# Performance work log

Measured on AMD Instinct MI355X. Metric: run time of the kernel, lower is better.

## Reference

```python
import jax, jax.numpy as jnp
import numpy as np

N_NODES = 100000
N_EDGES = 3200000
IN_CH = 512
OUT_CH = 64


def setup_inputs() -> dict:
    key = jax.random.key(0)
    k1, k2, k3 = jax.random.split(key, 3)
    edge_index = jax.random.randint(k1, (2, N_EDGES), 0, N_NODES, dtype=jnp.int64)
    x = jax.random.normal(k2, (N_NODES, IN_CH), dtype=jnp.float32)
    W = jax.random.normal(k3, (IN_CH, OUT_CH), dtype=jnp.float32)
    return {"edge_index": edge_index, "x": x, "W": W}


def _propagate(h, row, col, norm, self_norm):
    # one hop of normalized adjacency: (D^-1/2 (A+I) D^-1/2) @ h
    msg = jax.ops.segment_sum(norm[:, None] * h[col], row, num_segments=h.shape[0])
    return msg + self_norm[:, None] * h


def reference(edge_index, x, W):
    n = x.shape[0]
    row, col = edge_index[0], edge_index[1]
    # remove_self_loops then add_self_loops: mask out i==i edges, add identity
    loop_mask = (row != col).astype(x.dtype)
    deg = jax.ops.segment_sum(loop_mask, row, num_segments=n) + 1.0  # +1 self-loop
    dinv = jax.lax.rsqrt(deg)  # deg >= 1, never inf
    norm = dinv[row] * dinv[col] * loop_mask
    self_norm = dinv * dinv
    # A_hat^2 @ (x W) == A_hat @ (A_hat @ (x W)); avoids sparse-sparse matmul
    h = x @ W
    h = _propagate(h, row, col, norm, self_norm)
    h = _propagate(h, row, col, norm, self_norm)
    return h
```

## Files before the change

kernel.cpp:

```cpp
#include <hip/hip_runtime.h>
#include <hip/hip_bf16.h>


#define OUTC 64
#define INC 512
#define ELLW 72
#define RPB 128
#define NBUCK 782
#define PBLK 256
#define CAP 32
#define OVFCAP 65536

typedef short bf16x8 __attribute__((ext_vector_type(8)));
typedef float f32x4 __attribute__((ext_vector_type(4)));
typedef int i32x4 __attribute__((ext_vector_type(4)));

static __device__ inline short f2bf(float f) {
    union { __hip_bfloat16 b; short s; } u;
    u.b = __float2bfloat16(f);
    return u.s;
}
static __device__ inline float bf2f(unsigned short s) {
    union { float f; unsigned u; } v;
    v.u = ((unsigned)s) << 16;
    return v.f;
}

__global__ __launch_bounds__(1024) void bucket_scatter(const int* __restrict__ erow,
                                                       int* __restrict__ cnt_pb,
                                                       unsigned int* __restrict__ buf,
                                                       unsigned long long* __restrict__ ovf,
                                                       int* __restrict__ ovf_cnt,
                                                       int nE, int n) {
    __shared__ int lcnt[NBUCK];
    for (int i = threadIdx.x; i < NBUCK; i += 1024) lcnt[i] = 0;
    __syncthreads();
    const int blk = blockIdx.x;
    const int chunk = nE / PBLK;
    const int e0 = blk * chunk;
    const int e1 = (blk == PBLK - 1) ? nE : e0 + chunk;
    const int q0 = e0 >> 2, q1 = e1 >> 2;
    const i32x4* rows4 = (const i32x4*)erow;
    const i32x4* cols4 = (const i32x4*)(erow + nE);
    for (int q = q0 + (int)threadIdx.x; q < q1; q += 1024) {
        i32x4 r4 = __builtin_nontemporal_load(&rows4[q]);
        i32x4 c4 = __builtin_nontemporal_load(&cols4[q]);
#pragma unroll
        for (int k = 0; k < 4; ++k) {
            int r = r4[k], c = c4[k];
            if (r == c) continue;
            int b = r >> 7;
            int p = atomicAdd(&lcnt[b], 1);
            if (p < CAP) {
                buf[((size_t)b * PBLK + blk) * CAP + p] =
                    ((unsigned int)(r & (RPB - 1)) << 17) | (unsigned int)c;
            } else {
                int qq = atomicAdd(ovf_cnt, 1);
                if (qq < OVFCAP)
                    ovf[qq] = ((unsigned long long)(unsigned)r << 32) | (unsigned)c;
            }
        }
    }
    for (int e = (q1 << 2) + (int)threadIdx.x; e < e1; e += 1024) {
        int r = erow[e], c = erow[nE + e];
        if (r == c) continue;
        int b = r >> 7;
        int p = atomicAdd(&lcnt[b], 1);
        if (p < CAP) {
            buf[((size_t)b * PBLK + blk) * CAP + p] =
                ((unsigned int)(r & (RPB - 1)) << 17) | (unsigned int)c;
        } else {
            int qq = atomicAdd(ovf_cnt, 1);
            if (qq < OVFCAP)
                ovf[qq] = ((unsigned long long)(unsigned)r << 32) | (unsigned)c;
        }
    }
    __syncthreads();
    for (int i = threadIdx.x; i < NBUCK; i += 1024) {
        int v = lcnt[i];
        cnt_pb[(size_t)i * PBLK + blk] = v < CAP ? v : CAP;
    }
}

__global__ __launch_bounds__(256) void ell_from_buckets(const unsigned int* __restrict__ buf,
                                                        const int* __restrict__ cnt_pb,
                                                        const unsigned long long* __restrict__ ovf,
                                                        const int* __restrict__ ovf_cnt,
                                                        int* __restrict__ cnt,
                                                        float* __restrict__ dinv,
                                                        int* __restrict__ ell, int n) {
    __shared__ int segc[PBLK];
    __shared__ int rcnt[RPB];
    __shared__ int slab[RPB * ELLW];
    const int b = blockIdx.x;
    for (int i = threadIdx.x; i < PBLK; i += 256) segc[i] = cnt_pb[(size_t)b * PBLK + i];
    for (int i = threadIdx.x; i < RPB; i += 256) rcnt[i] = 0;
    __syncthreads();
    const unsigned int* bb = buf + (size_t)b * PBLK * CAP;
    const int TOT = PBLK * CAP;
    for (int j = threadIdx.x; j < TOT; j += 256) {
        int s = j >> 5;
        int off = j & (CAP - 1);
        if (off < segc[s]) {
            unsigned int u = bb[j];
            int lr = (int)(u >> 17);
            int c = (int)(u & 0x1FFFFu);
            int p = atomicAdd(&rcnt[lr], 1);
            if (p < ELLW) slab[lr * ELLW + p] = c;
        }
    }
    int m = *ovf_cnt;
    if (m > OVFCAP) m = OVFCAP;
    for (int i = threadIdx.x; i < m; i += 256) {
        unsigned long long e = ovf[i];
        int r = (int)(e >> 32);
        if ((r >> 7) == b) {
            int lr = r & (RPB - 1);
            int p = atomicAdd(&rcnt[lr], 1);
            if (p < ELLW) slab[lr * ELLW + p] = (int)(unsigned)(e & 0xFFFFFFFFu);
        }
    }
    __syncthreads();
    for (int lr = threadIdx.x; lr < RPB; lr += 256) {
        int r = b * RPB + lr;
        if (r < n) {
            int d = rcnt[lr];
            cnt[r] = d;
            dinv[r] = rsqrtf((float)d + 1.0f);
        }
    }
    int* dst = ell + (size_t)b * RPB * ELLW;
    for (int i = threadIdx.x; i < RPB * ELLW; i += 256) dst[i] = slab[i];
}

__global__ __launch_bounds__(256) void prep_w(const float* __restrict__ W,
                                              short* __restrict__ Whp,
                                              short* __restrict__ Wlp) {
    const int tid = blockIdx.x * 256 + threadIdx.x;
    const int lane = tid & 63;
    const int frag = tid >> 6;
    const int kt = frag >> 2;
    const int nt = frag & 3;
    const int col = nt * 16 + (lane & 15);
    const int kb = kt * 32 + (lane >> 4) * 8;
    short h8[8], l8[8];
#pragma unroll
    for (int j = 0; j < 8; ++j) {
        float w = W[(size_t)(kb + j) * OUTC + col];
        short wh = f2bf(w);
        h8[j] = wh;
        l8[j] = f2bf(w - bf2f((unsigned short)wh));
    }
    size_t o = ((size_t)frag * 64 + lane) * 8;
#pragma unroll
    for (int j = 0; j < 8; ++j) { Whp[o + j] = h8[j]; Wlp[o + j] = l8[j]; }
}

__global__ __launch_bounds__(256) void gemm_mfma(const float* __restrict__ x,
                                                 const short* __restrict__ Whp,
                                                 const short* __restrict__ Wlp,
                                                 const float* __restrict__ dinv,
                                                 unsigned short* __restrict__ h, int n) {
    const int lane = threadIdx.x & 63;
    const int wid = __builtin_amdgcn_readfirstlane(threadIdx.x >> 6);
    const int m0 = (blockIdx.x * 4 + wid) * 16;
    if (m0 >= n) return;
    const int quad = lane >> 4;
    const int row = m0 + (lane & 15);

    f32x4 acc[4];
#pragma unroll
    for (int nt = 0; nt < 4; ++nt) acc[nt] = (f32x4){0.f, 0.f, 0.f, 0.f};

    const float* xrow = x + (size_t)row * INC + quad * 8;

    for (int kt = 0; kt < 16; ++kt) {
        float4 a0 = *(const float4*)(xrow + kt * 32);
        float4 a1 = *(const float4*)(xrow + kt * 32 + 4);
        float av[8] = {a0.x, a0.y, a0.z, a0.w, a1.x, a1.y, a1.z, a1.w};
        bf16x8 ah, al;
#pragma unroll
        for (int j = 0; j < 8; ++j) {
            short hj = f2bf(av[j]);
            ah[j] = hj;
            al[j] = f2bf(av[j] - bf2f((unsigned short)hj));
        }
        const size_t fb = ((size_t)kt * 4 * 64 + lane) * 8;
#pragma unroll
        for (int nt = 0; nt < 4; ++nt) {
            bf16x8 bh = *(const bf16x8*)&Whp[fb + (size_t)nt * 64 * 8];
            bf16x8 bl = *(const bf16x8*)&Wlp[fb + (size_t)nt * 64 * 8];
            acc[nt] = __builtin_amdgcn_mfma_f32_16x16x32_bf16(ah, bh, acc[nt], 0, 0, 0);
            acc[nt] = __builtin_amdgcn_mfma_f32_16x16x32_bf16(ah, bl, acc[nt], 0, 0, 0);
            acc[nt] = __builtin_amdgcn_mfma_f32_16x16x32_bf16(al, bh, acc[nt], 0, 0, 0);
        }
    }
    float dv[4];
#pragma unroll
    for (int reg = 0; reg < 4; ++reg) dv[reg] = dinv[m0 + quad * 4 + reg];
#pragma unroll
    for (int nt = 0; nt < 4; ++nt) {
#pragma unroll
        for (int reg = 0; reg < 4; ++reg) {
            int crow = m0 + quad * 4 + reg;
            h[(size_t)crow * OUTC + nt * 16 + (lane & 15)] =
                (unsigned short)f2bf(dv[reg] * acc[nt][reg]);
        }
    }
}

__global__ __launch_bounds__(256) void prop_ell(const unsigned short* __restrict__ hs,
                                                void* __restrict__ hout,
                                                const int* __restrict__ cnt,
                                                const int* __restrict__ ell,
                                                const float* __restrict__ dinv,
                                                int n, int finalhop) {
    const int lane = threadIdx.x & 63;
    const int wid = __builtin_amdgcn_readfirstlane(threadIdx.x >> 6);
    const int node = blockIdx.x * 4 + wid;
    if (node >= n) return;
    float acc = bf2f(hs[(size_t)node * OUTC + lane]);
    int deg = cnt[node];
    if (deg > ELLW) deg = ELLW;
    const int* rowp = ell + (size_t)node * ELLW;
    int j = 0;
    for (; j + 16 <= deg; j += 16) {
        int4 c0 = *(const int4*)(rowp + j);
        int4 c1 = *(const int4*)(rowp + j + 4);
        int4 c2 = *(const int4*)(rowp + j + 8);
        int4 c3 = *(const int4*)(rowp + j + 12);
        float t0 = bf2f(hs[(size_t)c0.x * OUTC + lane]);
        float t1 = bf2f(hs[(size_t)c0.y * OUTC + lane]);
        float t2 = bf2f(hs[(size_t)c0.z * OUTC + lane]);
        float t3 = bf2f(hs[(size_t)c0.w * OUTC + lane]);
        float t4 = bf2f(hs[(size_t)c1.x * OUTC + lane]);
        float t5 = bf2f(hs[(size_t)c1.y * OUTC + lane]);
        float t6 = bf2f(hs[(size_t)c1.z * OUTC + lane]);
        float t7 = bf2f(hs[(size_t)c1.w * OUTC + lane]);
        float t8 = bf2f(hs[(size_t)c2.x * OUTC + lane]);
        float t9 = bf2f(hs[(size_t)c2.y * OUTC + lane]);
        float ta = bf2f(hs[(size_t)c2.z * OUTC + lane]);
        float tb = bf2f(hs[(size_t)c2.w * OUTC + lane]);
        float tc = bf2f(hs[(size_t)c3.x * OUTC + lane]);
        float td = bf2f(hs[(size_t)c3.y * OUTC + lane]);
        float te = bf2f(hs[(size_t)c3.z * OUTC + lane]);
        float tf = bf2f(hs[(size_t)c3.w * OUTC + lane]);
        acc += ((t0 + t1) + (t2 + t3)) + ((t4 + t5) + (t6 + t7));
        acc += ((t8 + t9) + (ta + tb)) + ((tc + td) + (te + tf));
    }
    for (; j + 4 <= deg; j += 4) {
        int4 c0 = *(const int4*)(rowp + j);
        float t0 = bf2f(hs[(size_t)c0.x * OUTC + lane]);
        float t1 = bf2f(hs[(size_t)c0.y * OUTC + lane]);
        float t2 = bf2f(hs[(size_t)c0.z * OUTC + lane]);
        float t3 = bf2f(hs[(size_t)c0.w * OUTC + lane]);
        acc += (t0 + t1) + (t2 + t3);
    }
    for (; j < deg; ++j) {
        int cc = rowp[j];
        acc += bf2f(hs[(size_t)cc * OUTC + lane]);
    }
    float di = dinv[node];
    if (finalhop) {
        ((float*)hout)[(size_t)node * OUTC + lane] = di * acc;
    } else {
        ((unsigned short*)hout)[(size_t)node * OUTC + lane] =
            (unsigned short)f2bf(di * di * acc);
    }
}

extern "C" void kernel_launch(void* const* d_in, const int* in_sizes, int n_in,
                              void* d_out, int out_size, void* d_ws, size_t ws_size,
                              hipStream_t stream) {
    const int n = out_size / OUTC;
    const int nE = in_sizes[0] / 2;
    const int* erow = (const int*)d_in[0];
    const float* x = (const float*)d_in[1];
    const float* W = (const float*)d_in[2];
    float* out = (float*)d_out;

    char* base = (char*)d_ws;
    size_t off = 0;
    auto take = [&](size_t nbytes) -> void* {
        void* p = base + off;
        off += (nbytes + 255) & ~(size_t)255;
        return p;
    };
    int* cnt = (int*)take((size_t)n * 4);
    float* dinv = (float*)take((size_t)n * 4);
    int* ell = (int*)take((size_t)NBUCK * RPB * ELLW * 4);
    short* Whp = (short*)take((size_t)INC * OUTC * 2);
    short* Wlp = (short*)take((size_t)INC * OUTC * 2);
    unsigned short* h0 = (unsigned short*)take((size_t)n * OUTC * 2);
    unsigned short* h1 = (unsigned short*)take((size_t)n * OUTC * 2);
    unsigned int* buf = (unsigned int*)take((size_t)NBUCK * PBLK * CAP * 4);
    int* cnt_pb = (int*)take((size_t)NBUCK * PBLK * 4);
    unsigned long long* ovf = (unsigned long long*)take((size_t)OVFCAP * 8);
    int* ovf_cnt = (int*)take(256);

    (void)hipMemsetAsync(ovf_cnt, 0, 4, stream);

    bucket_scatter<<<PBLK, 1024, 0, stream>>>(erow, cnt_pb, buf, ovf, ovf_cnt, nE, n);

    ell_from_buckets<<<NBUCK, 256, 0, stream>>>(buf, cnt_pb, ovf, ovf_cnt, cnt, dinv, ell, n);

    prep_w<<<16, 256, 0, stream>>>(W, Whp, Wlp);

    const int nwaves = (n + 15) / 16;
    gemm_mfma<<<(nwaves + 3) / 4, 256, 0, stream>>>(x, Whp, Wlp, dinv, h0, n);

    prop_ell<<<(n + 3) / 4, 256, 0, stream>>>(h0, (void*)h1, cnt, ell, dinv, n, 0);
    prop_ell<<<(n + 3) / 4, 256, 0, stream>>>(h1, (void*)out, cnt, ell, dinv, n, 1);
}
```

Before: 497.5 us.

## Partition propagation gather into column segments for cache locality

The ELL construction now sorts each row's neighbours into four source-node ranges and stores per-segment counts. Propagation runs as four passes per hop, each gathering only from one quarter of the feature rows so that pass's working set can stay in cache. Partial sums go to an fp32 accumulator buffer in global memory. This adds extra read-modify-write traffic on the accumulator, more kernel launches, and a second scan over the buckets during ELL construction.

```diff
diff --git a/kernel.cpp b/kernel.cpp
--- a/kernel.cpp
+++ b/kernel.cpp
@@ -10,6 +10,7 @@
 #define PBLK 256
 #define CAP 32
 #define OVFCAP 65536
+#define NSEG 4
 
 typedef short bf16x8 __attribute__((ext_vector_type(8)));
 typedef float f32x4 __attribute__((ext_vector_type(4)));
@@ -25,6 +26,7 @@
     v.u = ((unsigned)s) << 16;
     return v.f;
 }
+
 
 __global__ __launch_bounds__(1024) void bucket_scatter(const int* __restrict__ erow,
                                                        int* __restrict__ cnt_pb,
@@ -86,27 +88,28 @@
                                                         const int* __restrict__ cnt_pb,
                                                         const unsigned long long* __restrict__ ovf,
                                                         const int* __restrict__ ovf_cnt,
-                                                        int* __restrict__ cnt,
+                                                        int4* __restrict__ cnt4,
                                                         float* __restrict__ dinv,
-                                                        int* __restrict__ ell, int n) {
+                                                        int* __restrict__ ell,
+                                                        int n, int segw) {
     __shared__ int segc[PBLK];
-    __shared__ int rcnt[RPB];
+    __shared__ int scnt[RPB][NSEG];
+    __shared__ int soff[RPB][NSEG];
+    __shared__ int scur[RPB][NSEG];
     __shared__ int slab[RPB * ELLW];
     const int b = blockIdx.x;
     for (int i = threadIdx.x; i < PBLK; i += 256) segc[i] = cnt_pb[(size_t)b * PBLK + i];
-    for (int i = threadIdx.x; i < RPB; i += 256) rcnt[i] = 0;
+    for (int i = threadIdx.x; i < RPB * NSEG; i += 256) ((int*)scnt)[i] = 0;
     __syncthreads();
     const unsigned int* bb = buf + (size_t)b * PBLK * CAP;
     const int TOT = PBLK * CAP;
     for (int j = threadIdx.x; j < TOT; j += 256) {
-        int s = j >> 5;
-        int off = j & (CAP - 1);
+        int s = j >> 5, off = j & (CAP - 1);
         if (off < segc[s]) {
             unsigned int u = bb[j];
             int lr = (int)(u >> 17);
             int c = (int)(u & 0x1FFFFu);
-            int p = atomicAdd(&rcnt[lr], 1);
-            if (p < ELLW) slab[lr * ELLW + p] = c;
+            atomicAdd(&scnt[lr][c / segw], 1);
         }
     }
     int m = *ovf_cnt;
@@ -115,18 +118,61 @@
         unsigned long long e = ovf[i];
         int r = (int)(e >> 32);
         if ((r >> 7) == b) {
+            int c = (int)(unsigned)(e & 0xFFFFFFFFu);
+            atomicAdd(&scnt[r & (RPB - 1)][c / segw], 1);
+        }
+    }
+    __syncthreads();
+    for (int lr = threadIdx.x; lr < RPB; lr += 256) {
+        int o = 0;
+#pragma unroll
+        for (int s = 0; s < NSEG; ++s) {
+            soff[lr][s] = o < ELLW ? o : ELLW;
+            scur[lr][s] = 0;
+            o += scnt[lr][s];
+        }
+    }
+    __syncthreads();
+    for (int j = threadIdx.x; j < TOT; j += 256) {
+        int s = j >> 5, off = j & (CAP - 1);
+        if (off < segc[s]) {
+            unsigned int u = bb[j];
+            int lr = (int)(u >> 17);
+            int c = (int)(u & 0x1FFFFu);
+            int sg = c / segw;
+            int p = atomicAdd(&scur[lr][sg], 1);
+            int idx = soff[lr][sg] + p;
+            if (idx < ELLW) slab[lr * ELLW + idx] = c;
+        }
+    }
+    for (int i = threadIdx.x; i < m; i += 256) {
+        unsigned long long e = ovf[i];
+        int r = (int)(e >> 32);
+        if ((r >> 7) == b) {
             int lr = r & (RPB - 1);
-            int p = atomicAdd(&rcnt[lr], 1);
-            if (p < ELLW) slab[lr * ELLW + p] = (int)(unsigned)(e & 0xFFFFFFFFu);
+            int c = (int)(unsigned)(e & 0xFFFFFFFFu);
+            int sg = c / segw;
+            int p = atomicAdd(&scur[lr][sg], 1);
+            int idx = soff[lr][sg] + p;
+            if (idx < ELLW) slab[lr * ELLW + idx] = c;
         }
     }
     __syncthreads();
     for (int lr = threadIdx.x; lr < RPB; lr += 256) {
         int r = b * RPB + lr;
         if (r < n) {
-            int d = rcnt[lr];
-            cnt[r] = d;
-            dinv[r] = rsqrtf((float)d + 1.0f);
+            int raw = scnt[lr][0] + scnt[lr][1] + scnt[lr][2] + scnt[lr][3];
+            int pl[NSEG];
+#pragma unroll
+            for (int s = 0; s < NSEG; ++s) {
+                int start = soff[lr][s];
+                int avail = ELLW - start;
+                if (avail < 0) avail = 0;
+                int p = scnt[lr][s];
+                pl[s] = p < avail ? p : avail;
+            }
+            cnt4[r] = make_int4(pl[0], pl[1], pl[2], pl[3]);
+            dinv[r] = rsqrtf((float)raw + 1.0f);
         }
     }
     int* dst = ell + (size_t)b * RPB * ELLW;
@@ -156,6 +202,7 @@
     for (int j = 0; j < 8; ++j) { Whp[o + j] = h8[j]; Wlp[o + j] = l8[j]; }
 }
 
+
 __global__ __launch_bounds__(256) void gemm_mfma(const float* __restrict__ x,
                                                  const short* __restrict__ Whp,
                                                  const short* __restrict__ Wlp,
@@ -209,63 +256,54 @@
     }
 }
 
-__global__ __launch_bounds__(256) void prop_ell(const unsigned short* __restrict__ hs,
+__global__ __launch_bounds__(256) void prop_seg(const unsigned short* __restrict__ hs,
+                                                float* __restrict__ acc,
                                                 void* __restrict__ hout,
-                                                const int* __restrict__ cnt,
+                                                const int4* __restrict__ cnt4,
                                                 const int* __restrict__ ell,
                                                 const float* __restrict__ dinv,
-                                                int n, int finalhop) {
+                                                int n, int seg, int finalhop) {
     const int lane = threadIdx.x & 63;
     const int wid = __builtin_amdgcn_readfirstlane(threadIdx.x >> 6);
     const int node = blockIdx.x * 4 + wid;
     if (node >= n) return;
-    float acc = bf2f(hs[(size_t)node * OUTC + lane]);
-    int deg = cnt[node];
-    if (deg > ELLW) deg = ELLW;
-    const int* rowp = ell + (size_t)node * ELLW;
+    int4 c4 = cnt4[node];
+    int cs[4] = {c4.x, c4.y, c4.z, c4.w};
+    int start = 0;
+    for (int s = 0; s < seg; ++s) start += cs[s];
+    const int len = cs[seg];
+    const int* rowp = ell + (size_t)node * ELLW + start;
+    float a = 0.f;
     int j = 0;
-    for (; j + 16 <= deg; j += 16) {
-        int4 c0 = *(const int4*)(rowp + j);
-        int4 c1 = *(const int4*)(rowp + j + 4);
-        int4 c2 = *(const int4*)(rowp + j + 8);
-        int4 c3 = *(const int4*)(rowp + j + 12);
-        float t0 = bf2f(hs[(size_t)c0.x * OUTC + lane]);
-        float t1 = bf2f(hs[(size_t)c0.y * OUTC + lane]);
-        float t2 = bf2f(hs[(size_t)c0.z * OUTC + lane]);
-        float t3 = bf2f(hs[(size_t)c0.w * OUTC + lane]);
-        float t4 = bf2f(hs[(size_t)c1.x * OUTC + lane]);
-        float t5 = bf2f(hs[(size_t)c1.y * OUTC + lane]);
-        float t6 = bf2f(hs[(size_t)c1.z * OUTC + lane]);
-        float t7 = bf2f(hs[(size_t)c1.w * OUTC + lane]);
-        float t8 = bf2f(hs[(size_t)c2.x * OUTC + lane]);
-        float t9 = bf2f(hs[(size_t)c2.y * OUTC + lane]);
-        float ta = bf2f(hs[(size_t)c2.z * OUTC + lane]);
-        float tb = bf2f(hs[(size_t)c2.w * OUTC + lane]);
-        float tc = bf2f(hs[(size_t)c3.x * OUTC + lane]);
-        float td = bf2f(hs[(size_t)c3.y * OUTC + lane]);
-        float te = bf2f(hs[(size_t)c3.z * OUTC + lane]);
-        float tf = bf2f(hs[(size_t)c3.w * OUTC + lane]);
-        acc += ((t0 + t1) + (t2 + t3)) + ((t4 + t5) + (t6 + t7));
-        acc += ((t8 + t9) + (ta + tb)) + ((tc + td) + (te + tf));
-    }
-    for (; j + 4 <= deg; j += 4) {
-        int4 c0 = *(const int4*)(rowp + j);
-        float t0 = bf2f(hs[(size_t)c0.x * OUTC + lane]);
-        float t1 = bf2f(hs[(size_t)c0.y * OUTC + lane]);
-        float t2 = bf2f(hs[(size_t)c0.z * OUTC + lane]);
-        float t3 = bf2f(hs[(size_t)c0.w * OUTC + lane]);
-        acc += (t0 + t1) + (t2 + t3);
-    }
-    for (; j < deg; ++j) {
-        int cc = rowp[j];
-        acc += bf2f(hs[(size_t)cc * OUTC + lane]);
-    }
-    float di = dinv[node];
-    if (finalhop) {
-        ((float*)hout)[(size_t)node * OUTC + lane] = di * acc;
+    for (; j + 8 <= len; j += 8) {
+        int i0 = rowp[j], i1 = rowp[j + 1], i2 = rowp[j + 2], i3 = rowp[j + 3];
+        int i4 = rowp[j + 4], i5 = rowp[j + 5], i6 = rowp[j + 6], i7 = rowp[j + 7];
+        float t0 = bf2f(hs[(size_t)i0 * OUTC + lane]);
+        float t1 = bf2f(hs[(size_t)i1 * OUTC + lane]);
+        float t2 = bf2f(hs[(size_t)i2 * OUTC + lane]);
+        float t3 = bf2f(hs[(size_t)i3 * OUTC + lane]);
+        float t4 = bf2f(hs[(size_t)i4 * OUTC + lane]);
+        float t5 = bf2f(hs[(size_t)i5 * OUTC + lane]);
+        float t6 = bf2f(hs[(size_t)i6 * OUTC + lane]);
+        float t7 = bf2f(hs[(size_t)i7 * OUTC + lane]);
+        a += ((t0 + t1) + (t2 + t3)) + ((t4 + t5) + (t6 + t7));
+    }
+    for (; j < len; ++j)
+        a += bf2f(hs[(size_t)rowp[j] * OUTC + lane]);
+
+    const size_t oi = (size_t)node * OUTC + lane;
+    if (seg == 0) {
+        a += bf2f(hs[oi]);
+        acc[oi] = a;
+    } else if (seg < NSEG - 1) {
+        acc[oi] += a;
     } else {
-        ((unsigned short*)hout)[(size_t)node * OUTC + lane] =
-            (unsigned short)f2bf(di * di * acc);
+        float v = acc[oi] + a;
+        float di = dinv[node];
+        if (finalhop)
+            ((float*)hout)[oi] = di * v;
+        else
+            ((unsigned short*)hout)[oi] = (unsigned short)f2bf(di * di * v);
     }
 }
 
@@ -278,6 +316,7 @@
     const float* x = (const float*)d_in[1];
     const float* W = (const float*)d_in[2];
     float* out = (float*)d_out;
+    const int segw = (n + NSEG - 1) / NSEG;
 
     char* base = (char*)d_ws;
     size_t off = 0;
@@ -286,13 +325,14 @@
         off += (nbytes + 255) & ~(size_t)255;
         return p;
     };
-    int* cnt = (int*)take((size_t)n * 4);
+    int4* cnt4 = (int4*)take((size_t)n * 16);
     float* dinv = (float*)take((size_t)n * 4);
     int* ell = (int*)take((size_t)NBUCK * RPB * ELLW * 4);
     short* Whp = (short*)take((size_t)INC * OUTC * 2);
     short* Wlp = (short*)take((size_t)INC * OUTC * 2);
     unsigned short* h0 = (unsigned short*)take((size_t)n * OUTC * 2);
     unsigned short* h1 = (unsigned short*)take((size_t)n * OUTC * 2);
+    float* acc = (float*)take((size_t)n * OUTC * 4);
     unsigned int* buf = (unsigned int*)take((size_t)NBUCK * PBLK * CAP * 4);
     int* cnt_pb = (int*)take((size_t)NBUCK * PBLK * 4);
     unsigned long long* ovf = (unsigned long long*)take((size_t)OVFCAP * 8);
@@ -301,14 +341,16 @@
     (void)hipMemsetAsync(ovf_cnt, 0, 4, stream);
 
     bucket_scatter<<<PBLK, 1024, 0, stream>>>(erow, cnt_pb, buf, ovf, ovf_cnt, nE, n);
-
-    ell_from_buckets<<<NBUCK, 256, 0, stream>>>(buf, cnt_pb, ovf, ovf_cnt, cnt, dinv, ell, n);
-
+    ell_from_buckets<<<NBUCK, 256, 0, stream>>>(buf, cnt_pb, ovf, ovf_cnt, cnt4, dinv,
+                                                ell, n, segw);
     prep_w<<<16, 256, 0, stream>>>(W, Whp, Wlp);
 
     const int nwaves = (n + 15) / 16;
     gemm_mfma<<<(nwaves + 3) / 4, 256, 0, stream>>>(x, Whp, Wlp, dinv, h0, n);
 
-    prop_ell<<<(n + 3) / 4, 256, 0, stream>>>(h0, (void*)h1, cnt, ell, dinv, n, 0);
-    prop_ell<<<(n + 3) / 4, 256, 0, stream>>>(h1, (void*)out, cnt, ell, dinv, n, 1);
-}
+    const int pgrid = (n + 3) / 4;
+    for (int s = 0; s < NSEG; ++s)
+        prop_seg<<<pgrid, 256, 0, stream>>>(h0, acc, (void*)h1, cnt4, ell, dinv, n, s, 0);
+    for (int s = 0; s < NSEG; ++s)
+        prop_seg<<<pgrid, 256, 0, stream>>>(h1, acc, (void*)out, cnt4, ell, dinv, n, s, 1);
+}
```

Result: slower. 740.8 us (+48.9%).

## Co-schedule edge bucketing with the GEMM in one launch and defer dinv scaling

Applied to the files above, without the earlier changes.

The edge bucket scatter and the x@W MFMA GEMM now run as one kernel whose blocks split by index, so the atomic-bound scatter overlaps the bandwidth-bound GEMM. Because dinv is not known yet when the GEMM runs, the dinv row scaling of h0 moves into ell_from_buckets, which rescales each row slab in place after computing degrees. Nontemporal loads and stores are also added in the GEMM and propagation kernels. This costs an extra read-modify-write pass over h0 and a second bf16 rounding, and the scatter blocks drop from 1024 to 512 threads.

```diff
diff --git a/kernel.cpp b/kernel.cpp
--- a/kernel.cpp
+++ b/kernel.cpp
@@ -10,10 +10,12 @@
 #define PBLK 256
 #define CAP 32
 #define OVFCAP 65536
+#define GEMM_BLK 782
 
 typedef short bf16x8 __attribute__((ext_vector_type(8)));
 typedef float f32x4 __attribute__((ext_vector_type(4)));
 typedef int i32x4 __attribute__((ext_vector_type(4)));
+typedef unsigned short u16x4 __attribute__((ext_vector_type(4)));
 
 static __device__ inline short f2bf(float f) {
     union { __hip_bfloat16 b; short s; } u;
@@ -26,28 +28,71 @@
     return v.f;
 }
 
-__global__ __launch_bounds__(1024) void bucket_scatter(const int* __restrict__ erow,
-                                                       int* __restrict__ cnt_pb,
-                                                       unsigned int* __restrict__ buf,
-                                                       unsigned long long* __restrict__ ovf,
-                                                       int* __restrict__ ovf_cnt,
-                                                       int nE, int n) {
-    __shared__ int lcnt[NBUCK];
-    for (int i = threadIdx.x; i < NBUCK; i += 1024) lcnt[i] = 0;
-    __syncthreads();
-    const int blk = blockIdx.x;
-    const int chunk = nE / PBLK;
-    const int e0 = blk * chunk;
-    const int e1 = (blk == PBLK - 1) ? nE : e0 + chunk;
-    const int q0 = e0 >> 2, q1 = e1 >> 2;
-    const i32x4* rows4 = (const i32x4*)erow;
-    const i32x4* cols4 = (const i32x4*)(erow + nE);
-    for (int q = q0 + (int)threadIdx.x; q < q1; q += 1024) {
-        i32x4 r4 = __builtin_nontemporal_load(&rows4[q]);
-        i32x4 c4 = __builtin_nontemporal_load(&cols4[q]);
-#pragma unroll
-        for (int k = 0; k < 4; ++k) {
-            int r = r4[k], c = c4[k];
+__global__ __launch_bounds__(256) void prep_w(const float* __restrict__ W,
+                                              short* __restrict__ Whp,
+                                              short* __restrict__ Wlp) {
+    const int tid = blockIdx.x * 256 + threadIdx.x;
+    const int lane = tid & 63;
+    const int frag = tid >> 6;
+    const int kt = frag >> 2;
+    const int nt = frag & 3;
+    const int col = nt * 16 + (lane & 15);
+    const int kb = kt * 32 + (lane >> 4) * 8;
+    short h8[8], l8[8];
+#pragma unroll
+    for (int j = 0; j < 8; ++j) {
+        float w = W[(size_t)(kb + j) * OUTC + col];
+        short wh = f2bf(w);
+        h8[j] = wh;
+        l8[j] = f2bf(w - bf2f((unsigned short)wh));
+    }
+    size_t o = ((size_t)frag * 64 + lane) * 8;
+#pragma unroll
+    for (int j = 0; j < 8; ++j) { Whp[o + j] = h8[j]; Wlp[o + j] = l8[j]; }
+}
+
+__global__ __launch_bounds__(512) void scatter_and_gemm(const int* __restrict__ erow,
+                                                        int* __restrict__ cnt_pb,
+                                                        unsigned int* __restrict__ buf,
+                                                        unsigned long long* __restrict__ ovf,
+                                                        int* __restrict__ ovf_cnt,
+                                                        const float* __restrict__ x,
+                                                        const short* __restrict__ Whp,
+                                                        const short* __restrict__ Wlp,
+                                                        unsigned short* __restrict__ h,
+                                                        int nE, int n) {
+    if (blockIdx.x < PBLK) {
+        __shared__ int lcnt[NBUCK];
+        for (int i = threadIdx.x; i < NBUCK; i += 512) lcnt[i] = 0;
+        __syncthreads();
+        const int blk = blockIdx.x;
+        const int chunk = nE / PBLK;
+        const int e0 = blk * chunk;
+        const int e1 = (blk == PBLK - 1) ? nE : e0 + chunk;
+        const int q0 = e0 >> 2, q1 = e1 >> 2;
+        const i32x4* rows4 = (const i32x4*)erow;
+        const i32x4* cols4 = (const i32x4*)(erow + nE);
+        for (int q = q0 + (int)threadIdx.x; q < q1; q += 512) {
+            i32x4 r4 = __builtin_nontemporal_load(&rows4[q]);
+            i32x4 c4 = __builtin_nontemporal_load(&cols4[q]);
+#pragma unroll
+            for (int k = 0; k < 4; ++k) {
+                int r = r4[k], c = c4[k];
+                if (r == c) continue;
+                int b = r >> 7;
+                int p = atomicAdd(&lcnt[b], 1);
+                if (p < CAP) {
+                    buf[((size_t)b * PBLK + blk) * CAP + p] =
+                        ((unsigned int)(r & (RPB - 1)) << 17) | (unsigned int)c;
+                } else {
+                    int qq = atomicAdd(ovf_cnt, 1);
+                    if (qq < OVFCAP)
+                        ovf[qq] = ((unsigned long long)(unsigned)r << 32) | (unsigned)c;
+                }
+            }
+        }
+        for (int e = (q1 << 2) + (int)threadIdx.x; e < e1; e += 512) {
+            int r = erow[e], c = erow[nE + e];
             if (r == c) continue;
             int b = r >> 7;
             int p = atomicAdd(&lcnt[b], 1);
@@ -60,25 +105,56 @@
                     ovf[qq] = ((unsigned long long)(unsigned)r << 32) | (unsigned)c;
             }
         }
-    }
-    for (int e = (q1 << 2) + (int)threadIdx.x; e < e1; e += 1024) {
-        int r = erow[e], c = erow[nE + e];
-        if (r == c) continue;
-        int b = r >> 7;
-        int p = atomicAdd(&lcnt[b], 1);
-        if (p < CAP) {
-            buf[((size_t)b * PBLK + blk) * CAP + p] =
-                ((unsigned int)(r & (RPB - 1)) << 17) | (unsigned int)c;
-        } else {
-            int qq = atomicAdd(ovf_cnt, 1);
-            if (qq < OVFCAP)
-                ovf[qq] = ((unsigned long long)(unsigned)r << 32) | (unsigned)c;
-        }
-    }
-    __syncthreads();
-    for (int i = threadIdx.x; i < NBUCK; i += 1024) {
-        int v = lcnt[i];
-        cnt_pb[(size_t)i * PBLK + blk] = v < CAP ? v : CAP;
+        __syncthreads();
+        for (int i = threadIdx.x; i < NBUCK; i += 512) {
+            int v = lcnt[i];
+            cnt_pb[(size_t)i * PBLK + blk] = v < CAP ? v : CAP;
+        }
+        return;
+    }
+    const int lane = threadIdx.x & 63;
+    const int wid = __builtin_amdgcn_readfirstlane(threadIdx.x >> 6);
+    const int slab = (blockIdx.x - PBLK) * 8 + wid;
+    const int m0 = slab * 16;
+    if (m0 >= n) return;
+    const int quad = lane >> 4;
+    const int row = m0 + (lane & 15);
+
+    f32x4 acc[4];
+#pragma unroll
+    for (int nt = 0; nt < 4; ++nt) acc[nt] = (f32x4){0.f, 0.f, 0.f, 0.f};
+
+    const float* xrow = x + (size_t)row * INC + quad * 8;
+
+    for (int kt = 0; kt < 16; ++kt) {
+        f32x4 a0 = __builtin_nontemporal_load((const f32x4*)(xrow + kt * 32));
+        f32x4 a1 = __builtin_nontemporal_load((const f32x4*)(xrow + kt * 32 + 4));
+        float av[8] = {a0[0], a0[1], a0[2], a0[3], a1[0], a1[1], a1[2], a1[3]};
+        bf16x8 ah, al;
+#pragma unroll
+        for (int j = 0; j < 8; ++j) {
+            short hj = f2bf(av[j]);
+            ah[j] = hj;
+            al[j] = f2bf(av[j] - bf2f((unsigned short)hj));
+        }
+        const size_t fb = ((size_t)kt * 4 * 64 + lane) * 8;
+#pragma unroll
+        for (int nt = 0; nt < 4; ++nt) {
+            bf16x8 bh = *(const bf16x8*)&Whp[fb + (size_t)nt * 64 * 8];
+            bf16x8 bl = *(const bf16x8*)&Wlp[fb + (size_t)nt * 64 * 8];
+            acc[nt] = __builtin_amdgcn_mfma_f32_16x16x32_bf16(ah, bh, acc[nt], 0, 0, 0);
+            acc[nt] = __builtin_amdgcn_mfma_f32_16x16x32_bf16(ah, bl, acc[nt], 0, 0, 0);
+            acc[nt] = __builtin_amdgcn_mfma_f32_16x16x32_bf16(al, bh, acc[nt], 0, 0, 0);
+        }
+    }
+#pragma unroll
+    for (int nt = 0; nt < 4; ++nt) {
+#pragma unroll
+        for (int reg = 0; reg < 4; ++reg) {
+            int crow = m0 + quad * 4 + reg;
+            h[(size_t)crow * OUTC + nt * 16 + (lane & 15)] =
+                (unsigned short)f2bf(acc[nt][reg]);
+        }
     }
 }
 
@@ -88,9 +164,12 @@
                                                         const int* __restrict__ ovf_cnt,
                                                         int* __restrict__ cnt,
                                                         float* __restrict__ dinv,
-                                                        int* __restrict__ ell, int n) {
+                                                        int* __restrict__ ell,
+                                                        unsigned short* __restrict__ h0,
+                                                        int n) {
     __shared__ int segc[PBLK];
     __shared__ int rcnt[RPB];
+    __shared__ float sdinv[RPB];
     __shared__ int slab[RPB * ELLW];
     const int b = blockIdx.x;
     for (int i = threadIdx.x; i < PBLK; i += 256) segc[i] = cnt_pb[(size_t)b * PBLK + i];
@@ -125,88 +204,33 @@
         int r = b * RPB + lr;
         if (r < n) {
             int d = rcnt[lr];
+            float dv = rsqrtf((float)d + 1.0f);
             cnt[r] = d;
-            dinv[r] = rsqrtf((float)d + 1.0f);
+            dinv[r] = dv;
+            sdinv[lr] = dv;
+        }
+    }
+    __syncthreads();
+    {
+        const int r0 = b * RPB;
+        int nr = n - r0;
+        if (nr > RPB) nr = RPB;
+        if (nr > 0) {
+            u16x4* hv = (u16x4*)(h0 + (size_t)r0 * OUTC);
+            const int nchunk = nr * (OUTC / 4);
+            for (int i = threadIdx.x; i < nchunk; i += 256) {
+                float dv = sdinv[i >> 4];
+                u16x4 v = hv[i];
+                u16x4 o;
+#pragma unroll
+                for (int j = 0; j < 4; ++j)
+                    o[j] = (unsigned short)f2bf(dv * bf2f(v[j]));
+                hv[i] = o;
+            }
         }
     }
     int* dst = ell + (size_t)b * RPB * ELLW;
     for (int i = threadIdx.x; i < RPB * ELLW; i += 256) dst[i] = slab[i];
-}
-
-__global__ __launch_bounds__(256) void prep_w(const float* __restrict__ W,
-                                              short* __restrict__ Whp,
-                                              short* __restrict__ Wlp) {
-    const int tid = blockIdx.x * 256 + threadIdx.x;
-    const int lane = tid & 63;
-    const int frag = tid >> 6;
-    const int kt = frag >> 2;
-    const int nt = frag & 3;
-    const int col = nt * 16 + (lane & 15);
-    const int kb = kt * 32 + (lane >> 4) * 8;
-    short h8[8], l8[8];
-#pragma unroll
-    for (int j = 0; j < 8; ++j) {
-        float w = W[(size_t)(kb + j) * OUTC + col];
-        short wh = f2bf(w);
-        h8[j] = wh;
-        l8[j] = f2bf(w - bf2f((unsigned short)wh));
-    }
-    size_t o = ((size_t)frag * 64 + lane) * 8;
-#pragma unroll
-    for (int j = 0; j < 8; ++j) { Whp[o + j] = h8[j]; Wlp[o + j] = l8[j]; }
-}
-
-__global__ __launch_bounds__(256) void gemm_mfma(const float* __restrict__ x,
-                                                 const short* __restrict__ Whp,
-                                                 const short* __restrict__ Wlp,
-                                                 const float* __restrict__ dinv,
-                                                 unsigned short* __restrict__ h, int n) {
-    const int lane = threadIdx.x & 63;
-    const int wid = __builtin_amdgcn_readfirstlane(threadIdx.x >> 6);
-    const int m0 = (blockIdx.x * 4 + wid) * 16;
-    if (m0 >= n) return;
-    const int quad = lane >> 4;
-    const int row = m0 + (lane & 15);
-
-    f32x4 acc[4];
-#pragma unroll
-    for (int nt = 0; nt < 4; ++nt) acc[nt] = (f32x4){0.f, 0.f, 0.f, 0.f};
-
-    const float* xrow = x + (size_t)row * INC + quad * 8;
-
-    for (int kt = 0; kt < 16; ++kt) {
-        float4 a0 = *(const float4*)(xrow + kt * 32);
-        float4 a1 = *(const float4*)(xrow + kt * 32 + 4);
-        float av[8] = {a0.x, a0.y, a0.z, a0.w, a1.x, a1.y, a1.z, a1.w};
-        bf16x8 ah, al;
-#pragma unroll
-        for (int j = 0; j < 8; ++j) {
-            short hj = f2bf(av[j]);
-            ah[j] = hj;
-            al[j] = f2bf(av[j] - bf2f((unsigned short)hj));
-        }
-        const size_t fb = ((size_t)kt * 4 * 64 + lane) * 8;
-#pragma unroll
-        for (int nt = 0; nt < 4; ++nt) {
-            bf16x8 bh = *(const bf16x8*)&Whp[fb + (size_t)nt * 64 * 8];
-            bf16x8 bl = *(const bf16x8*)&Wlp[fb + (size_t)nt * 64 * 8];
-            acc[nt] = __builtin_amdgcn_mfma_f32_16x16x32_bf16(ah, bh, acc[nt], 0, 0, 0);
-            acc[nt] = __builtin_amdgcn_mfma_f32_16x16x32_bf16(ah, bl, acc[nt], 0, 0, 0);
-            acc[nt] = __builtin_amdgcn_mfma_f32_16x16x32_bf16(al, bh, acc[nt], 0, 0, 0);
-        }
-    }
-    float dv[4];
-#pragma unroll
-    for (int reg = 0; reg < 4; ++reg) dv[reg] = dinv[m0 + quad * 4 + reg];
-#pragma unroll
-    for (int nt = 0; nt < 4; ++nt) {
-#pragma unroll
-        for (int reg = 0; reg < 4; ++reg) {
-            int crow = m0 + quad * 4 + reg;
-            h[(size_t)crow * OUTC + nt * 16 + (lane & 15)] =
-                (unsigned short)f2bf(dv[reg] * acc[nt][reg]);
-        }
-    }
 }
 
 __global__ __launch_bounds__(256) void prop_ell(const unsigned short* __restrict__ hs,
@@ -225,35 +249,35 @@
     const int* rowp = ell + (size_t)node * ELLW;
     int j = 0;
     for (; j + 16 <= deg; j += 16) {
-        int4 c0 = *(const int4*)(rowp + j);
-        int4 c1 = *(const int4*)(rowp + j + 4);
-        int4 c2 = *(const int4*)(rowp + j + 8);
-        int4 c3 = *(const int4*)(rowp + j + 12);
-        float t0 = bf2f(hs[(size_t)c0.x * OUTC + lane]);
-        float t1 = bf2f(hs[(size_t)c0.y * OUTC + lane]);
-        float t2 = bf2f(hs[(size_t)c0.z * OUTC + lane]);
-        float t3 = bf2f(hs[(size_t)c0.w * OUTC + lane]);
-        float t4 = bf2f(hs[(size_t)c1.x * OUTC + lane]);
-        float t5 = bf2f(hs[(size_t)c1.y * OUTC + lane]);
-        float t6 = bf2f(hs[(size_t)c1.z * OUTC + lane]);
-        float t7 = bf2f(hs[(size_t)c1.w * OUTC + lane]);
-        float t8 = bf2f(hs[(size_t)c2.x * OUTC + lane]);
-        float t9 = bf2f(hs[(size_t)c2.y * OUTC + lane]);
-        float ta = bf2f(hs[(size_t)c2.z * OUTC + lane]);
-        float tb = bf2f(hs[(size_t)c2.w * OUTC + lane]);
-        float tc = bf2f(hs[(size_t)c3.x * OUTC + lane]);
-        float td = bf2f(hs[(size_t)c3.y * OUTC + lane]);
-        float te = bf2f(hs[(size_t)c3.z * OUTC + lane]);
-        float tf = bf2f(hs[(size_t)c3.w * OUTC + lane]);
+        i32x4 c0 = __builtin_nontemporal_load((const i32x4*)(rowp + j));
+        i32x4 c1 = __builtin_nontemporal_load((const i32x4*)(rowp + j + 4));
+        i32x4 c2 = __builtin_nontemporal_load((const i32x4*)(rowp + j + 8));
+        i32x4 c3 = __builtin_nontemporal_load((const i32x4*)(rowp + j + 12));
+        float t0 = bf2f(hs[(size_t)c0[0] * OUTC + lane]);
+        float t1 = bf2f(hs[(size_t)c0[1] * OUTC + lane]);
+        float t2 = bf2f(hs[(size_t)c0[2] * OUTC + lane]);
+        float t3 = bf2f(hs[(size_t)c0[3] * OUTC + lane]);
+        float t4 = bf2f(hs[(size_t)c1[0] * OUTC + lane]);
+        float t5 = bf2f(hs[(size_t)c1[1] * OUTC + lane]);
+        float t6 = bf2f(hs[(size_t)c1[2] * OUTC + lane]);
+        float t7 = bf2f(hs[(size_t)c1[3] * OUTC + lane]);
+        float t8 = bf2f(hs[(size_t)c2[0] * OUTC + lane]);
+        float t9 = bf2f(hs[(size_t)c2[1] * OUTC + lane]);
+        float ta = bf2f(hs[(size_t)c2[2] * OUTC + lane]);
+        float tb = bf2f(hs[(size_t)c2[3] * OUTC + lane]);
+        float tc = bf2f(hs[(size_t)c3[0] * OUTC + lane]);
+        float td = bf2f(hs[(size_t)c3[1] * OUTC + lane]);
+        float te = bf2f(hs[(size_t)c3[2] * OUTC + lane]);
+        float tf = bf2f(hs[(size_t)c3[3] * OUTC + lane]);
         acc += ((t0 + t1) + (t2 + t3)) + ((t4 + t5) + (t6 + t7));
         acc += ((t8 + t9) + (ta + tb)) + ((tc + td) + (te + tf));
     }
     for (; j + 4 <= deg; j += 4) {
-        int4 c0 = *(const int4*)(rowp + j);
-        float t0 = bf2f(hs[(size_t)c0.x * OUTC + lane]);
-        float t1 = bf2f(hs[(size_t)c0.y * OUTC + lane]);
-        float t2 = bf2f(hs[(size_t)c0.z * OUTC + lane]);
-        float t3 = bf2f(hs[(size_t)c0.w * OUTC + lane]);
+        i32x4 c0 = __builtin_nontemporal_load((const i32x4*)(rowp + j));
+        float t0 = bf2f(hs[(size_t)c0[0] * OUTC + lane]);
+        float t1 = bf2f(hs[(size_t)c0[1] * OUTC + lane]);
+        float t2 = bf2f(hs[(size_t)c0[2] * OUTC + lane]);
+        float t3 = bf2f(hs[(size_t)c0[3] * OUTC + lane]);
         acc += (t0 + t1) + (t2 + t3);
     }
     for (; j < deg; ++j) {
@@ -261,11 +285,12 @@
         acc += bf2f(hs[(size_t)cc * OUTC + lane]);
     }
     float di = dinv[node];
+    const size_t oi = (size_t)node * OUTC + lane;
     if (finalhop) {
-        ((float*)hout)[(size_t)node * OUTC + lane] = di * acc;
+        __builtin_nontemporal_store(di * acc, (float*)hout + oi);
     } else {
-        ((unsigned short*)hout)[(size_t)node * OUTC + lane] =
-            (unsigned short)f2bf(di * di * acc);
+        __builtin_nontemporal_store((unsigned short)f2bf(di * di * acc),
+                                    (unsigned short*)hout + oi);
     }
 }
 
@@ -300,15 +325,16 @@
 
     (void)hipMemsetAsync(ovf_cnt, 0, 4, stream);
 
-    bucket_scatter<<<PBLK, 1024, 0, stream>>>(erow, cnt_pb, buf, ovf, ovf_cnt, nE, n);
-
-    ell_from_buckets<<<NBUCK, 256, 0, stream>>>(buf, cnt_pb, ovf, ovf_cnt, cnt, dinv, ell, n);
-
     prep_w<<<16, 256, 0, stream>>>(W, Whp, Wlp);
 
-    const int nwaves = (n + 15) / 16;
-    gemm_mfma<<<(nwaves + 3) / 4, 256, 0, stream>>>(x, Whp, Wlp, dinv, h0, n);
-
-    prop_ell<<<(n + 3) / 4, 256, 0, stream>>>(h0, (void*)h1, cnt, ell, dinv, n, 0);
-    prop_ell<<<(n + 3) / 4, 256, 0, stream>>>(h1, (void*)out, cnt, ell, dinv, n, 1);
-}
+    scatter_and_gemm<<<PBLK + GEMM_BLK, 512, 0, stream>>>(erow, cnt_pb, buf, ovf,
+                                                          ovf_cnt, x, Whp, Wlp, h0,
+                                                          nE, n);
+
+    ell_from_buckets<<<NBUCK, 256, 0, stream>>>(buf, cnt_pb, ovf, ovf_cnt, cnt, dinv,
+                                                ell, h0, n);
+
+    const int pgrid = (n + 3) / 4;
+    prop_ell<<<pgrid, 256, 0, stream>>>(h0, (void*)h1, cnt, ell, dinv, n, 0);
+    prop_ell<<<pgrid, 256, 0, stream>>>(h1, (void*)out, cnt, ell, dinv, n, 1);
+}
```

Result: slower. 523.3 us (+5.2%).
